# Kernel tuning notes

Hardware: AMD Instinct MI355X
Metric: run time of the kernel (lower is better)

Reference implementation:

```python
import jax, jax.numpy as jnp
import numpy as np
import math

B, N, D, H, L, F, K = 4, 256, 768, 32, 12, 3072, 128
HD = D // H
ATOM_TYPES = 64
EDGE_TYPES = ATOM_TYPES * ATOM_TYPES
BLOCKS = 1
SQRT_2PI = math.sqrt(2.0 * math.pi)


def _ln(x, g, b):
    m = jnp.mean(x, -1, keepdims=True)
    v = jnp.mean((x - m) ** 2, -1, keepdims=True)
    return (x - m) * jax.lax.rsqrt(v + 1e-5) * g + b


def _gelu(x):
    return jax.nn.gelu(x, approximate=False)


def setup_inputs():
    key = jax.random.key(0)
    ks = iter(jax.random.split(key, 64))
    def nrm(shape, s=0.02):
        return jax.random.normal(next(ks), shape, jnp.float32) * s
    inp = dict(
        atoms=jax.random.randint(next(ks), (B, N), 0, ATOM_TYPES),
        tags=jax.random.randint(next(ks), (B, N), 0, 3),
        pos=jax.random.normal(next(ks), (B, N, 3), jnp.float32) * 3.0,
        real_mask=jnp.ones((B, N), dtype=bool),
        atom_emb=nrm((ATOM_TYPES, D)),
        tag_emb=nrm((3, D)),
        gbf_means=jax.random.uniform(next(ks), (K,), jnp.float32, 0.0, 3.0),
        gbf_stds=jax.random.uniform(next(ks), (K,), jnp.float32, 0.0, 3.0),
        gbf_mul=jnp.ones((EDGE_TYPES, 1), jnp.float32),
        gbf_bias=jnp.zeros((EDGE_TYPES, 1), jnp.float32),
        bp_w1=nrm((K, K)), bp_b1=jnp.zeros((K,), jnp.float32),
        bp_w2=nrm((H, K)), bp_b2=jnp.zeros((H,), jnp.float32),
        ep_w=nrm((D, K)), ep_b=jnp.zeros((D,), jnp.float32),
        ln1_g=jnp.ones((L, D), jnp.float32), ln1_b=jnp.zeros((L, D), jnp.float32),
        wqkv=nrm((L, 3 * D, D)), bqkv=jnp.zeros((L, 3 * D), jnp.float32),
        wo=nrm((L, D, D)), bo=jnp.zeros((L, D), jnp.float32),
        ln2_g=jnp.ones((L, D), jnp.float32), ln2_b=jnp.zeros((L, D), jnp.float32),
        w1=nrm((L, F, D)), b1=jnp.zeros((L, F), jnp.float32),
        w2=nrm((L, D, F)), b2=jnp.zeros((L, D), jnp.float32),
        fln_g=jnp.ones((D,), jnp.float32), fln_b=jnp.zeros((D,), jnp.float32),
        en_w1=nrm((D, D)), en_b1=jnp.zeros((D,), jnp.float32),
        en_w2=nrm((1, D)), en_b2=jnp.zeros((1,), jnp.float32),
        eagg=nrm((3, 1), 0.01),
        nq_w=nrm((D, D)), nq_b=jnp.zeros((D,), jnp.float32),
        nk_w=nrm((D, D)), nk_b=jnp.zeros((D,), jnp.float32),
        nv_w=nrm((D, D)), nv_b=jnp.zeros((D,), jnp.float32),
        f1_w=nrm((1, D)), f1_b=jnp.zeros((1,), jnp.float32),
        f2_w=nrm((1, D)), f2_b=jnp.zeros((1,), jnp.float32),
        f3_w=nrm((1, D)), f3_b=jnp.zeros((1,), jnp.float32),
    )
    return inp


def _forward(atoms, tags, real_mask, pos, atom_emb, tag_emb, gbf_means, gbf_stds, gbf_mul, gbf_bias,
             bp_w1, bp_b1, bp_w2, bp_b2, ep_w, ep_b,
             ln1_g, ln1_b, wqkv, bqkv, wo, bo, ln2_g, ln2_b, w1, b1, w2, b2,
             fln_g, fln_b, en_w1, en_b1, en_w2, en_b2, eagg,
             nq_w, nq_b, nk_w, nk_b, nv_w, nv_b, f1_w, f1_b, f2_w, f2_b, f3_w, f3_b):
    pad = atoms == 0                                              # [B,N]
    # delta[b,i,j] = pos[b,j] - pos[b,i]  (matches pos.unsqueeze(1) - pos.unsqueeze(2))
    delta = pos[:, None, :, :] - pos[:, :, None, :]               # [B,N,N,3]
    sq = jnp.sum(delta * delta, axis=-1)
    dist = jnp.sqrt(jnp.maximum(sq, 1e-24))                       # safe norm, zero grad on diagonal
    delta = delta / (dist[..., None] + 1e-5)
    edge_type = atoms[:, :, None] * ATOM_TYPES + atoms[:, None, :]  # [B,N,N]
    # Gaussian basis layer
    mul = gbf_mul[edge_type]                                      # [B,N,N,1]
    add = gbf_bias[edge_type]                                     # [B,N,N,1]
    x = mul * dist[..., None] + add                               # [B,N,N,1] -> broadcast to K
    std = jnp.abs(gbf_stds) + 1e-5                                # [K]
    z = (x - gbf_means) / std
    gbf = jnp.exp(-0.5 * z * z) / (SQRT_2PI * std)                # [B,N,N,K]
    edge_feat = jnp.where(pad[:, None, :, None], 0.0, gbf)
    node = tag_emb[tags] + atom_emb[atoms] + (edge_feat.sum(-2) @ ep_w.T + ep_b)  # [B,N,D]
    bias = _gelu(gbf @ bp_w1.T + bp_b1) @ bp_w2.T + bp_b2         # [B,N,N,H]
    bias = jnp.transpose(bias, (0, 3, 1, 2))                      # [B,H,N,N]
    bias = jnp.where(pad[:, None, None, :], -jnp.inf, bias)
    scale = HD ** -0.5
    h = node
    for _ in range(BLOCKS):
        for l in range(L):
            r = h
            y = _ln(h, ln1_g[l], ln1_b[l])
            qkv = y @ wqkv[l].T + bqkv[l]
            q, k, v = jnp.split(qkv, 3, axis=-1)
            q = q.reshape(B, N, H, HD).transpose(0, 2, 1, 3) * scale
            k = k.reshape(B, N, H, HD).transpose(0, 2, 1, 3)
            v = v.reshape(B, N, H, HD).transpose(0, 2, 1, 3)
            a = jnp.einsum('bhid,bhjd->bhij', q, k) + bias
            a = jax.nn.softmax(a, axis=-1)
            o = jnp.einsum('bhij,bhjd->bhid', a, v).transpose(0, 2, 1, 3).reshape(B, N, D)
            h = r + (o @ wo[l].T + bo[l])
            r = h
            y = _ln(h, ln2_g[l], ln2_b[l])
            y = _gelu(y @ w1[l].T + b1[l]) @ w2[l].T + b2[l]
            h = r + y
    out = _ln(h, fln_g, fln_b)                                    # [B,N,D]
    # energy head (eval: no dropout)
    eng = _gelu(out @ en_w1.T + en_b1) @ en_w2.T + en_b2          # [B,N,1]
    eng = (eng * eagg[tags])[..., 0]                              # [B,N]
    omask = (tags > 0) & real_mask
    eng_output = (eng * omask).sum(-1)                            # [B]
    # node task head
    q = (out @ nq_w.T + nq_b).reshape(B, N, H, HD).transpose(0, 2, 1, 3) * scale
    k = (out @ nk_w.T + nk_b).reshape(B, N, H, HD).transpose(0, 2, 1, 3)
    v = (out @ nv_w.T + nv_b).reshape(B, N, H, HD).transpose(0, 2, 1, 3)
    a = jnp.einsum('bhid,bhjd->bhij', q, k) + bias
    a = jax.nn.softmax(a, axis=-1)                                # [B,H,N,N]
    # rot_attn_probs @ v, fused: [b,h,i,j]*[b,i,j,c]*[b,h,j,d] -> [b,i,c,h,d]
    xf = jnp.einsum('bhij,bijc,bhjd->bichd', a, delta, v).reshape(B, N, 3, D)
    f1 = xf[:, :, 0] @ f1_w.T + f1_b
    f2 = xf[:, :, 1] @ f2_w.T + f2_b
    f3 = xf[:, :, 2] @ f3_w.T + f3_b
    node_output = jnp.concatenate([f1, f2, f3], axis=-1)          # [B,N,3]
    return eng_output, node_output, omask[..., None]


def reference(atoms, tags, pos, real_mask, atom_emb, tag_emb, gbf_means, gbf_stds, gbf_mul, gbf_bias,
              bp_w1, bp_b1, bp_w2, bp_b2, ep_w, ep_b,
              ln1_g, ln1_b, wqkv, bqkv, wo, bo, ln2_g, ln2_b, w1, b1, w2, b2,
              fln_g, fln_b, en_w1, en_b1, en_w2, en_b2, eagg,
              nq_w, nq_b, nk_w, nk_b, nv_w, nv_b, f1_w, f1_b, f2_w, f2_b, f3_w, f3_b):
    return _forward(atoms, tags, real_mask, pos, atom_emb, tag_emb, gbf_means, gbf_stds, gbf_mul, gbf_bias,
                    bp_w1, bp_b1, bp_w2, bp_b2, ep_w, ep_b,
                    ln1_g, ln1_b, wqkv, bqkv, wo, bo, ln2_g, ln2_b, w1, b1, w2, b2,
                    fln_g, fln_b, en_w1, en_b1, en_w2, en_b2, eagg,
                    nq_w, nq_b, nk_w, nk_b, nv_w, nv_b, f1_w, f1_b, f2_w, f2_b, f3_w, f3_b)
```

## Files before the change

kernel.cpp:

```cpp
#include <hip/hip_runtime.h>
#include <math.h>

constexpr int B_ = 4, N_ = 256, D_ = 768, H_ = 32, HD_ = 24, L_ = 12, F_ = 3072, K_ = 128;
constexpr float SCALE_ = 0.20412414523193150f;
constexpr float ISQRT2_ = 0.70710678118654752f;

typedef short bf16x8 __attribute__((ext_vector_type(8)));
typedef float f32x4 __attribute__((ext_vector_type(4)));
typedef unsigned short u16x4 __attribute__((ext_vector_type(4)));
typedef unsigned short u16x8 __attribute__((ext_vector_type(8)));
typedef unsigned int u32x4 __attribute__((ext_vector_type(4)));

#define DEV __device__ __forceinline__
#define MFMA16(a, b, c) __builtin_amdgcn_mfma_f32_16x16x32_bf16(a, b, c, 0, 0, 0)

DEV void gload_lds16(const unsigned short* g, unsigned short* l) {
  __builtin_amdgcn_global_load_lds(
      (const __attribute__((address_space(1))) unsigned int*)(g),
      (__attribute__((address_space(3))) unsigned int*)(l), 16, 0, 0);
}

DEV float gelu_f(float x) { return 0.5f * x * (1.0f + erff(x * ISQRT2_)); }

DEV unsigned short f2bf(float f) {
  unsigned u = __float_as_uint(f);
  return (unsigned short)((u + 0x7FFFu + ((u >> 16) & 1u)) >> 16);
}
DEV float bf2f(unsigned short u) { return __uint_as_float(((unsigned)u) << 16); }
DEV unsigned packbf(float a, float b) {
  return (unsigned)f2bf(a) | ((unsigned)f2bf(b) << 16);
}
DEV bf16x8 u4_to_bf8(u32x4 x) { union { u32x4 a; bf16x8 b; } u; u.a = x; return u.b; }

DEV float breduce_sum(float v, float* sred, int tid) {
#pragma unroll
  for (int o = 32; o > 0; o >>= 1) v += __shfl_xor(v, o);
  if ((tid & 63) == 0) sred[tid >> 6] = v;
  __syncthreads();
  v = (sred[0] + sred[1]) + (sred[2] + sred[3]);
  __syncthreads();
  return v;
}

__global__ __launch_bounds__(256) void cast_one_kernel(
    const float* __restrict__ s, unsigned short* __restrict__ d, int n4) {
  const int i = blockIdx.x * 256 + threadIdx.x;
  if (i >= n4) return;
  const float4 v = ((const float4*)s)[i];
  u16x4 o = {f2bf(v.x), f2bf(v.y), f2bf(v.z), f2bf(v.w)};
  ((u16x4*)d)[i] = o;
}

__global__ __launch_bounds__(256) void castlayer_kernel(
    const float* __restrict__ wqkv, const float* __restrict__ wo,
    const float* __restrict__ w1, const float* __restrict__ w2,
    unsigned short* __restrict__ arena) {
  const int i = blockIdx.x * 256 + threadIdx.x;
  const float* s; int j;
  if (i < 442368) { s = wqkv; j = i; }
  else if (i < 589824) { s = wo; j = i - 442368; }
  else if (i < 1179648) { s = w1; j = i - 589824; }
  else { s = w2; j = i - 1179648; }
  const float4 v = ((const float4*)s)[j];
  u16x4 o = {f2bf(v.x), f2bf(v.y), f2bf(v.z), f2bf(v.w)};
  ((u16x4*)arena)[i] = o;
}

__global__ __launch_bounds__(256) void castheads_kernel(
    const float* __restrict__ a, const float* __restrict__ b,
    const float* __restrict__ c, const float* __restrict__ d,
    unsigned short* __restrict__ arena) {
  const int i = blockIdx.x * 256 + threadIdx.x;
  const int r = i / 147456;
  const int j = i - r * 147456;
  const float* s = (r == 0) ? a : (r == 1) ? b : (r == 2) ? c : d;
  const float4 v = ((const float4*)s)[j];
  u16x4 o = {f2bf(v.x), f2bf(v.y), f2bf(v.z), f2bf(v.w)};
  ((u16x4*)arena)[i] = o;
}

__global__ __launch_bounds__(256) void edge_pre_kernel(
    const int* __restrict__ atoms, const float* __restrict__ pos,
    const float* __restrict__ gbf_mul, const float* __restrict__ gbf_bias,
    const float* __restrict__ gbf_means, const float* __restrict__ gbf_stds,
    float* __restrict__ deltaw, float* __restrict__ xvalw, float* __restrict__ nsumw)
{
  const int tid = threadIdx.x;
  const int bi = blockIdx.x;
  const int b = bi >> 8;
  __shared__ float spos[3];
  __shared__ float sxv[256];
  __shared__ int   spad[256];
  __shared__ float red[256];
  if (tid < 3) spos[tid] = pos[(size_t)bi * 3 + tid];
  __syncthreads();
  {
    const int j = tid;
    const float px = pos[(size_t)(b * N_ + j) * 3 + 0];
    const float py = pos[(size_t)(b * N_ + j) * 3 + 1];
    const float pz = pos[(size_t)(b * N_ + j) * 3 + 2];
    const float dx = px - spos[0], dy = py - spos[1], dz = pz - spos[2];
    const float sq = dx * dx + dy * dy + dz * dz;
    const float dist = sqrtf(fmaxf(sq, 1e-24f));
    const float inv = 1.f / (dist + 1e-5f);
    const size_t e = (size_t)bi * N_ + j;
    deltaw[e * 3 + 0] = dx * inv;
    deltaw[e * 3 + 1] = dy * inv;
    deltaw[e * 3 + 2] = dz * inv;
    const int et = atoms[bi] * 64 + atoms[b * N_ + j];
    const float xv = gbf_mul[et] * dist + gbf_bias[et];
    xvalw[e] = xv;
    sxv[j] = xv;
    spad[j] = (atoms[b * N_ + j] == 0);
  }
  __syncthreads();
  const int k = tid & 127;
  const float mean = gbf_means[k];
  const float st = fabsf(gbf_stds[k]) + 1e-5f;
  const float istd = 1.f / st;
  const float coef = 0.39894228040143268f * istd;
  float acc = 0.f;
  const int jbase = tid >> 7;
  for (int t = 0; t < 128; ++t) {
    const int j = jbase + (t << 1);
    if (!spad[j]) {
      const float z = (sxv[j] - mean) * istd;
      acc += expf(-0.5f * z * z) * coef;
    }
  }
  red[tid] = acc;
  __syncthreads();
  if (tid < 128) nsumw[(size_t)bi * K_ + tid] = red[tid] + red[tid + 128];
}

__global__ __launch_bounds__(256) void bias_mfma_kernel(
    const float* __restrict__ xvalw, const int* __restrict__ atoms,
    const float* __restrict__ gbf_means, const float* __restrict__ gbf_stds,
    const unsigned short* __restrict__ w1b, const float* __restrict__ b1,
    const unsigned short* __restrict__ w2b, const float* __restrict__ b2,
    unsigned short* __restrict__ biasb)
{
  __shared__ __align__(16) unsigned short sw1[128 * 128];
  __shared__ __align__(16) unsigned short sw2[32 * 128];
  __shared__ float smean[128], sistd[128], scoef[128], sb1[128], sb2[32];
  const int tid = threadIdx.x;
  const int l = tid & 63;
  const int w = tid >> 6;
  const size_t e0 = (size_t)blockIdx.x * 64;
  const int bB = (int)(e0 >> 16);
  const int iI = (int)((e0 >> 8) & 255);
  const int j0 = (int)(e0 & 255);
  const int lr = l & 15;
  const int lg = l >> 4;

  {
    const int rin = l >> 4;
    const int slot = l & 15;
#pragma unroll
    for (int q = 0; q < 8; ++q) {
      const int rbase = w * 32 + q * 4;
      const int row = rbase + rin;
      const int gs = slot ^ (row & 15);
      gload_lds16(w1b + row * 128 + gs * 8, &sw1[rbase * 128]);
    }
#pragma unroll
    for (int q = 0; q < 2; ++q) {
      const int rbase = w * 8 + q * 4;
      const int row = rbase + rin;
      const int gs = slot ^ (row & 15);
      gload_lds16(w2b + row * 128 + gs * 8, &sw2[rbase * 128]);
    }
  }
  if (tid < 128) {
    const float st = fabsf(gbf_stds[tid]) + 1e-5f;
    const float is = 1.f / st;
    smean[tid] = gbf_means[tid];
    sistd[tid] = is;
    scoef[tid] = 0.39894228040143268f * is;
    sb1[tid] = b1[tid];
  } else if (tid < 160) {
    sb2[tid - 128] = b2[tid - 128];
  }
  const int el = w * 16 + lr;
  const float xv = xvalw[e0 + el];
  const bool padq = (atoms[bB * N_ + j0 + el] == 0);
  __syncthreads();

  bf16x8 bG[4];
#pragma unroll
  for (int ks = 0; ks < 4; ++ks) {
    u16x8 t;
#pragma unroll
    for (int j = 0; j < 8; ++j) {
      const int k = ks * 32 + lg * 8 + j;
      const float z = (xv - smean[k]) * sistd[k];
      t[j] = f2bf(__expf(-0.5f * z * z) * scoef[k]);
    }
    union { u16x8 a; bf16x8 b; } u; u.a = t;
    bG[ks] = u.b;
  }

  f32x4 accM[8];
#pragma unroll
  for (int f = 0; f < 8; ++f) accM[f] = (f32x4)0.f;
#pragma unroll
  for (int ks = 0; ks < 4; ++ks) {
#pragma unroll
    for (int f = 0; f < 8; ++f) {
      const int row = f * 16 + lr;
      const int sl = (ks * 4 + lg) ^ (row & 15);
      const bf16x8 aW = *(const bf16x8*)&sw1[row * 128 + (sl << 3)];
      accM[f] = MFMA16(aW, bG[ks], accM[f]);
    }
  }

  unsigned pm[8][2];
#pragma unroll
  for (int f = 0; f < 8; ++f) {
    float g[4];
#pragma unroll
    for (int r = 0; r < 4; ++r)
      g[r] = gelu_f(accM[f][r] + sb1[f * 16 + lg * 4 + r]);
    pm[f][0] = packbf(g[0], g[1]);
    pm[f][1] = packbf(g[2], g[3]);
  }

  f32x4 accH[2];
  accH[0] = (f32x4)0.f; accH[1] = (f32x4)0.f;
#pragma unroll
  for (int ks = 0; ks < 4; ++ks) {
    const int s0 = ((((lg << 1)) & 3) << 4) + lr;
    const int s1 = ((((lg << 1) + 1) & 3) << 4) + lr;
    const int sel = lg >> 1;
    const unsigned a0 = __shfl(pm[2 * ks][0], s0), b0 = __shfl(pm[2 * ks + 1][0], s0);
    const unsigned a1 = __shfl(pm[2 * ks][1], s0), b1v = __shfl(pm[2 * ks + 1][1], s0);
    const unsigned a2 = __shfl(pm[2 * ks][0], s1), b2v = __shfl(pm[2 * ks + 1][0], s1);
    const unsigned a3 = __shfl(pm[2 * ks][1], s1), b3v = __shfl(pm[2 * ks + 1][1], s1);
    u32x4 bw;
    bw.x = sel ? b0 : a0;
    bw.y = sel ? b1v : a1;
    bw.z = sel ? b2v : a2;
    bw.w = sel ? b3v : a3;
    const bf16x8 bMid = u4_to_bf8(bw);
#pragma unroll
    for (int hf = 0; hf < 2; ++hf) {
      const int row = hf * 16 + lr;
      const int sl = (ks * 4 + lg) ^ (row & 15);
      const bf16x8 aW2 = *(const bf16x8*)&sw2[row * 128 + (sl << 3)];
      accH[hf] = MFMA16(aW2, bMid, accH[hf]);
    }
  }

  const size_t obase = (((size_t)bB * H_) * N_ + iI) * N_ + j0 + el;
#pragma unroll
  for (int hf = 0; hf < 2; ++hf) {
#pragma unroll
    for (int r = 0; r < 4; ++r) {
      const int h = hf * 16 + lg * 4 + r;
      const unsigned short v = padq ? (unsigned short)0xFF80
                                    : f2bf(accH[hf][r] + sb2[h]);
      biasb[obase + (size_t)h * N_ * N_] = v;
    }
  }
}

__global__ __launch_bounds__(256) void node_init_kernel(
    const int* __restrict__ atoms, const int* __restrict__ tags,
    const float* __restrict__ atom_emb, const float* __restrict__ tag_emb,
    const float* __restrict__ nsumw, const float* __restrict__ ep_w,
    const float* __restrict__ ep_b, float* __restrict__ hbuf)
{
  const int bi = blockIdx.x;
  const int tid = threadIdx.x;
  __shared__ float ns[K_];
  if (tid < K_) ns[tid] = nsumw[(size_t)bi * K_ + tid];
  __syncthreads();
  const int at = atoms[bi], tg = tags[bi];
  for (int d = tid; d < D_; d += 256) {
    float acc = tag_emb[tg * D_ + d] + atom_emb[at * D_ + d] + ep_b[d];
    const float* w = ep_w + (size_t)d * K_;
#pragma unroll 8
    for (int kk = 0; kk < K_; ++kk) acc = fmaf(ns[kk], w[kk], acc);
    hbuf[(size_t)bi * D_ + d] = acc;
  }
}

__global__ __launch_bounds__(256) void ln_kernel(
    const float* __restrict__ x, const float* __restrict__ gg,
    const float* __restrict__ bb, unsigned short* __restrict__ y)
{
  const int bi = blockIdx.x;
  const int tid = threadIdx.x;
  __shared__ float sred[4];
  const float* row = x + (size_t)bi * D_;
  const float v0 = row[tid], v1 = row[tid + 256], v2 = row[tid + 512];
  float s = breduce_sum(v0 + v1 + v2, sred, tid);
  const float mean = s * (1.f / 768.f);
  const float d0 = v0 - mean, d1 = v1 - mean, d2 = v2 - mean;
  float q = breduce_sum(d0 * d0 + d1 * d1 + d2 * d2, sred, tid);
  const float inv = rsqrtf(q * (1.f / 768.f) + 1e-5f);
  unsigned short* out = y + (size_t)bi * D_;
  out[tid]       = f2bf(d0 * inv * gg[tid]       + bb[tid]);
  out[tid + 256] = f2bf(d1 * inv * gg[tid + 256] + bb[tid + 256]);
  out[tid + 512] = f2bf(d2 * inv * gg[tid + 512] + bb[tid + 512]);
}

template <int S>
__global__ __launch_bounds__(256) void reduce_ln_kernel(
    const float* __restrict__ P, const float* __restrict__ bias,
    float* __restrict__ hbuf, const float* __restrict__ gg,
    const float* __restrict__ bb, unsigned short* __restrict__ y)
{
  const int row = blockIdx.x;
  const int tid = threadIdx.x;
  __shared__ float sred[4];
  float h[3];
#pragma unroll
  for (int t = 0; t < 3; ++t) {
    const int c = tid + (t << 8);
    float s = bias[c];
#pragma unroll
    for (int z = 0; z < S; ++z)
      s += P[((size_t)z * (B_ * N_) + row) * 768 + c];
    const float hv = hbuf[(size_t)row * 768 + c] + s;
    hbuf[(size_t)row * 768 + c] = hv;
    h[t] = hv;
  }
  float sm = breduce_sum(h[0] + h[1] + h[2], sred, tid);
  const float mean = sm * (1.f / 768.f);
  const float d0 = h[0] - mean, d1 = h[1] - mean, d2 = h[2] - mean;
  float q = breduce_sum(d0 * d0 + d1 * d1 + d2 * d2, sred, tid);
  const float inv = rsqrtf(q * (1.f / 768.f) + 1e-5f);
  unsigned short* out = y + (size_t)row * 768;
  out[tid]       = f2bf(d0 * inv * gg[tid]       + bb[tid]);
  out[tid + 256] = f2bf(d1 * inv * gg[tid + 256] + bb[tid + 256]);
  out[tid + 512] = f2bf(d2 * inv * gg[tid + 512] + bb[tid + 512]);
}

template <int EPI, int OB>
__global__ __launch_bounds__(256) void gemm_mfma(
    const unsigned short* __restrict__ A, const unsigned short* __restrict__ W,
    const float* __restrict__ bias, const float* __restrict__ bias2,
    const float* __restrict__ bias3, const float* __restrict__ bias4,
    float* __restrict__ C, unsigned short* __restrict__ Cb,
    int M, int N, int K, int lda, int ldw)
{
  if (EPI == 4) {
    const int z = blockIdx.z;
    A += (size_t)z * K;
    W += (size_t)z * K;
    C += (size_t)z * M * N;
  }
  __shared__ __align__(16) unsigned short sA[2][64 * 64];
  __shared__ __align__(16) unsigned short sB[2][64 * 64];
  const int tid = threadIdx.x;
  const int l = tid & 63;
  const int w = tid >> 6;
  const int m0 = blockIdx.y * 64;
  const int n0 = blockIdx.x * 64;
  const int wm = w >> 1, wn = w & 1;
  const int lr = l & 15;
  const int lg = l >> 4;
  const int r0 = (w << 4) + (l >> 3);
  const int s0 = (l & 7) ^ (r0 & 7);

  f32x4 acc[2][2];
#pragma unroll
  for (int mi = 0; mi < 2; ++mi)
#pragma unroll
    for (int ni = 0; ni < 2; ++ni) acc[mi][ni] = (f32x4)0.f;

  auto stage = [&](int buf, int t) {
    const size_t kb = (size_t)t << 6;
    unsigned short* lA = &sA[buf][(w << 4) << 6];
    unsigned short* lB = &sB[buf][(w << 4) << 6];
    gload_lds16(A + (size_t)(m0 + r0) * lda + kb + (s0 << 3), lA);
    gload_lds16(A + (size_t)(m0 + r0 + 8) * lda + kb + (s0 << 3), lA + 8 * 64);
    gload_lds16(W + (size_t)(n0 + r0) * ldw + kb + (s0 << 3), lB);
    gload_lds16(W + (size_t)(n0 + r0 + 8) * ldw + kb + (s0 << 3), lB + 8 * 64);
  };

  stage(0, 0);
  const int nt = K >> 6;
  for (int t = 0; t < nt; ++t) {
    __syncthreads();
    if (t + 1 < nt) stage((t + 1) & 1, t + 1);
    const unsigned short* bA = sA[t & 1];
    const unsigned short* bBs = sB[t & 1];
    bf16x8 af[2][2], bfr[2][2];
#pragma unroll
    for (int mi = 0; mi < 2; ++mi) {
      const int row = (wm << 5) + (mi << 4) + lr;
#pragma unroll
      for (int kk = 0; kk < 2; ++kk) {
        const int sl = ((kk << 2) + lg) ^ (row & 7);
        af[mi][kk] = *(const bf16x8*)&bA[(row << 6) + (sl << 3)];
      }
    }
#pragma unroll
    for (int ni = 0; ni < 2; ++ni) {
      const int row = (wn << 5) + (ni << 4) + lr;
#pragma unroll
      for (int kk = 0; kk < 2; ++kk) {
        const int sl = ((kk << 2) + lg) ^ (row & 7);
        bfr[ni][kk] = *(const bf16x8*)&bBs[(row << 6) + (sl << 3)];
      }
    }
#pragma unroll
    for (int kk = 0; kk < 2; ++kk)
#pragma unroll
      for (int mi = 0; mi < 2; ++mi)
#pragma unroll
        for (int ni = 0; ni < 2; ++ni)
          acc[mi][ni] = MFMA16(af[mi][kk], bfr[ni][kk], acc[mi][ni]);
  }

#pragma unroll
  for (int mi = 0; mi < 2; ++mi)
#pragma unroll
    for (int ni = 0; ni < 2; ++ni) {
      const int n = n0 + (wn << 5) + (ni << 4) + lr;
      float bv = 0.f;
      int seg = 0;
      if (EPI == 3) {
        seg = n / 768;
        const float* bp = (seg == 0) ? bias : (seg == 1) ? bias2
                         : (seg == 2) ? bias3 : bias4;
        bv = bp[n - seg * 768];
      } else if (EPI != 4) {
        bv = bias[n];
      }
#pragma unroll
      for (int r = 0; r < 4; ++r) {
        const int m = m0 + (wm << 5) + (mi << 4) + lg * 4 + r;
        float v = acc[mi][ni][r] + bv;
        if (EPI == 1) v = gelu_f(v);
        if (EPI == 3 && seg == 3) v = gelu_f(v);
        if (OB) Cb[(size_t)m * N + n] = f2bf(v);
        else C[(size_t)m * N + n] = v;
      }
    }
}

template <bool PROBS>
__global__ __launch_bounds__(256) void attn_mfma_kernel(
    const unsigned short* __restrict__ Q, const unsigned short* __restrict__ Kp,
    const unsigned short* __restrict__ Vp, const int stride,
    const unsigned short* __restrict__ biasb, unsigned short* __restrict__ obuf,
    unsigned short* __restrict__ aprob)
{
  __shared__ __align__(16) unsigned short sK[256 * 40];
  __shared__ __align__(16) unsigned short sVt[32 * 264];
  __shared__ __align__(16) unsigned short sP[64 * 264];
  const int tid = threadIdx.x;
  const int l = tid & 63, w = tid >> 6;
  const int bh = blockIdx.x, b = bh >> 5, hh = bh & 31;
  const int i0 = blockIdx.y * 64;
  const int lr = l & 15, lg = l >> 4;

#pragma unroll
  for (int it = 0; it < 3; ++it) {
    const int c = tid + (it << 8);
    const int row = c / 3, part = c - row * 3;
    *(u16x8*)&sK[row * 40 + part * 8] =
        *(const u16x8*)&Kp[(size_t)(b * N_ + row) * stride + hh * HD_ + part * 8];
  }
  {
    u16x8 z = {0, 0, 0, 0, 0, 0, 0, 0};
    *(u16x8*)&sK[tid * 40 + 24] = z;
  }
  if (!PROBS) {
    const int j = tid;
    const unsigned short* vr = &Vp[(size_t)(b * N_ + j) * stride + hh * HD_];
    const u16x8 v0 = *(const u16x8*)vr;
    const u16x8 v1 = *(const u16x8*)(vr + 8);
    const u16x8 v2 = *(const u16x8*)(vr + 16);
#pragma unroll
    for (int d = 0; d < 8; ++d) {
      sVt[d * 264 + j] = v0[d];
      sVt[(8 + d) * 264 + j] = v1[d];
      sVt[(16 + d) * 264 + j] = v2[d];
    }
  }
  bf16x8 aQ;
  if (lg < 3) {
    const u16x8 q = *(const u16x8*)&Q[(size_t)(b * N_ + i0 + (w << 4) + lr) * stride + hh * HD_ + lg * 8];
    union { u16x8 a; bf16x8 b; } u; u.a = q;
    aQ = u.b;
  } else {
    bf16x8 t = {0, 0, 0, 0, 0, 0, 0, 0};
    aQ = t;
  }
  __syncthreads();

  f32x4 acc[16];
#pragma unroll
  for (int ni = 0; ni < 16; ++ni) {
    const bf16x8 bK = *(const bf16x8*)&sK[(ni * 16 + lr) * 40 + lg * 8];
    acc[ni] = MFMA16(aQ, bK, (f32x4)0.f);
  }

#pragma unroll
  for (int r = 0; r < 4; ++r) {
    const int iloc = (w << 4) + lg * 4 + r;
    const unsigned short* bp =
        &biasb[(((size_t)(b * H_ + hh)) * N_ + i0 + iloc) * N_ + lr];
    float mx = -INFINITY;
#pragma unroll
    for (int ni = 0; ni < 16; ++ni) {
      const float s = acc[ni][r] * SCALE_ + bf2f(bp[ni * 16]);
      acc[ni][r] = s;
      mx = fmaxf(mx, s);
    }
    mx = fmaxf(mx, __shfl_xor(mx, 1));
    mx = fmaxf(mx, __shfl_xor(mx, 2));
    mx = fmaxf(mx, __shfl_xor(mx, 4));
    mx = fmaxf(mx, __shfl_xor(mx, 8));
    float sum = 0.f;
#pragma unroll
    for (int ni = 0; ni < 16; ++ni) {
      const float e = expf(acc[ni][r] - mx);
      acc[ni][r] = e;
      sum += e;
    }
    sum += __shfl_xor(sum, 1);
    sum += __shfl_xor(sum, 2);
    sum += __shfl_xor(sum, 4);
    sum += __shfl_xor(sum, 8);
    const float inv = 1.f / sum;
#pragma unroll
    for (int ni = 0; ni < 16; ++ni)
      sP[iloc * 264 + ni * 16 + lr] = f2bf(acc[ni][r] * inv);
  }
  __syncthreads();

  if (PROBS) {
#pragma unroll
    for (int it = 0; it < 8; ++it) {
      const int idx = tid + it * 256;
      const int row = idx >> 5, c = idx & 31;
      *(u16x8*)&aprob[(((size_t)(b * H_ + hh)) * N_ + i0 + row) * N_ + c * 8] =
          *(const u16x8*)&sP[row * 264 + c * 8];
    }
  } else {
    f32x4 accO[2];
    accO[0] = (f32x4)0.f; accO[1] = (f32x4)0.f;
#pragma unroll
    for (int ks = 0; ks < 8; ++ks) {
      const bf16x8 aP = *(const bf16x8*)&sP[((w << 4) + lr) * 264 + ks * 32 + lg * 8];
      const bf16x8 bV0 = *(const bf16x8*)&sVt[lr * 264 + ks * 32 + lg * 8];
      const bf16x8 bV1 = *(const bf16x8*)&sVt[(16 + lr) * 264 + ks * 32 + lg * 8];
      accO[0] = MFMA16(aP, bV0, accO[0]);
      accO[1] = MFMA16(aP, bV1, accO[1]);
    }
#pragma unroll
    for (int ni = 0; ni < 2; ++ni) {
      const int n = ni * 16 + lr;
      if (n < HD_) {
#pragma unroll
        for (int r = 0; r < 4; ++r) {
          const int i = i0 + (w << 4) + lg * 4 + r;
          obuf[(size_t)(b * N_ + i) * D_ + hh * HD_ + n] = f2bf(accO[ni][r]);
        }
      }
    }
  }
}

__global__ __launch_bounds__(256) void engnode_kernel(
    const unsigned short* __restrict__ t1, const int stride,
    const float* __restrict__ en_w2, const float* __restrict__ en_b2,
    const float* __restrict__ eagg, const int* __restrict__ tags,
    float* __restrict__ engpn)
{
  const int bi = blockIdx.x;
  const int tid = threadIdx.x;
  __shared__ float sred[4];
  const unsigned short* row = t1 + (size_t)bi * stride;
  float acc = bf2f(row[tid]) * en_w2[tid] + bf2f(row[tid + 256]) * en_w2[tid + 256] +
              bf2f(row[tid + 512]) * en_w2[tid + 512];
  acc = breduce_sum(acc, sred, tid);
  if (tid == 0) {
    const int tg = tags[bi];
    engpn[bi] = (tg > 0) ? (acc + en_b2[0]) * eagg[tg] : 0.f;
  }
}

__global__ __launch_bounds__(256) void engsum_omask_kernel(
    const float* __restrict__ engpn, const int* __restrict__ tags,
    float* __restrict__ out)
{
  const int bid = blockIdx.x;
  const int tid = threadIdx.x;
  if (bid < 4) {
    __shared__ float sred[4];
    float v = breduce_sum(engpn[bid * N_ + tid], sred, tid);
    if (tid == 0) out[bid] = v;
  } else {
    const int idx = (bid - 4) * 256 + tid;
    out[4 + B_ * N_ * 3 + idx] = (tags[idx] > 0) ? 1.f : 0.f;
  }
}

__global__ __launch_bounds__(256) void wv_kernel(
    const unsigned short* __restrict__ vn, const int stride,
    const float* __restrict__ f1w, const float* __restrict__ f2w,
    const float* __restrict__ f3w, float* __restrict__ wv)
{
  const int idx = blockIdx.x * 256 + threadIdx.x;
  const int j = idx & 255;
  const int hh = (idx >> 8) & 31;
  const int b = (idx >> 13) & 3;
  const int c = idx >> 15;
  const float* fw = (c == 0) ? f1w : ((c == 1) ? f2w : f3w);
  const unsigned short* vrow = vn + (size_t)(b * N_ + j) * stride + hh * HD_;
  const u16x8 v0 = *(const u16x8*)vrow;
  const u16x8 v1 = *(const u16x8*)(vrow + 8);
  const u16x8 v2 = *(const u16x8*)(vrow + 16);
  float acc = 0.f;
#pragma unroll
  for (int d = 0; d < 8; ++d) {
    acc = fmaf(bf2f(v0[d]), fw[hh * HD_ + d], acc);
    acc = fmaf(bf2f(v1[d]), fw[hh * HD_ + 8 + d], acc);
    acc = fmaf(bf2f(v2[d]), fw[hh * HD_ + 16 + d], acc);
  }
  wv[idx] = acc;
}

__global__ __launch_bounds__(256) void nodeout_kernel(
    const unsigned short* __restrict__ aprob, const float* __restrict__ wv,
    const float* __restrict__ deltaw, const float* __restrict__ f1b,
    const float* __restrict__ f2b, const float* __restrict__ f3b,
    float* __restrict__ out)
{
  const int bi = blockIdx.x;
  const int c = blockIdx.y;
  const int tid = threadIdx.x;
  const int b = bi >> 8;
  const int i = bi & 255;
  __shared__ float sred[4];
  const unsigned short* ap = aprob + (((size_t)b * H_) * N_ + i) * N_ + tid;
  const float* wvp = wv + ((size_t)(c * B_ + b) * H_) * N_ + tid;
  float s = 0.f;
  for (int hh = 0; hh < H_; ++hh)
    s = fmaf(bf2f(ap[(size_t)hh * N_ * N_]), wvp[(size_t)hh * N_], s);
  s *= deltaw[((size_t)bi * N_ + tid) * 3 + c];
  s = breduce_sum(s, sred, tid);
  if (tid == 0) {
    const float fb = (c == 0) ? f1b[0] : ((c == 1) ? f2b[0] : f3b[0]);
    out[4 + bi * 3 + c] = s + fb;
  }
}

extern "C" void kernel_launch(void* const* d_in, const int* in_sizes, int n_in,
                              void* d_out, int out_size, void* d_ws, size_t ws_size,
                              hipStream_t stream) {
  (void)in_sizes; (void)n_in; (void)out_size; (void)ws_size;
  const int*   atoms     = (const int*)  d_in[0];
  const int*   tags      = (const int*)  d_in[1];
  const float* pos       = (const float*)d_in[2];
  const float* atom_emb  = (const float*)d_in[4];
  const float* tag_emb   = (const float*)d_in[5];
  const float* gbf_means = (const float*)d_in[6];
  const float* gbf_stds  = (const float*)d_in[7];
  const float* gbf_mul   = (const float*)d_in[8];
  const float* gbf_bias  = (const float*)d_in[9];
  const float* bp_w1     = (const float*)d_in[10];
  const float* bp_b1     = (const float*)d_in[11];
  const float* bp_w2     = (const float*)d_in[12];
  const float* bp_b2     = (const float*)d_in[13];
  const float* ep_w      = (const float*)d_in[14];
  const float* ep_b      = (const float*)d_in[15];
  const float* ln1_g     = (const float*)d_in[16];
  const float* ln1_b     = (const float*)d_in[17];
  const float* wqkv      = (const float*)d_in[18];
  const float* bqkv      = (const float*)d_in[19];
  const float* wo        = (const float*)d_in[20];
  const float* bo        = (const float*)d_in[21];
  const float* ln2_g     = (const float*)d_in[22];
  const float* ln2_b     = (const float*)d_in[23];
  const float* w1        = (const float*)d_in[24];
  const float* b1        = (const float*)d_in[25];
  const float* w2        = (const float*)d_in[26];
  const float* b2        = (const float*)d_in[27];
  const float* fln_g     = (const float*)d_in[28];
  const float* fln_b     = (const float*)d_in[29];
  const float* en_w1     = (const float*)d_in[30];
  const float* en_b1     = (const float*)d_in[31];
  const float* en_w2     = (const float*)d_in[32];
  const float* en_b2     = (const float*)d_in[33];
  const float* eagg      = (const float*)d_in[34];
  const float* nq_w      = (const float*)d_in[35];
  const float* nq_b      = (const float*)d_in[36];
  const float* nk_w      = (const float*)d_in[37];
  const float* nk_b      = (const float*)d_in[38];
  const float* nv_w      = (const float*)d_in[39];
  const float* nv_b      = (const float*)d_in[40];
  const float* f1_w      = (const float*)d_in[41];
  const float* f1_b      = (const float*)d_in[42];
  const float* f2_w      = (const float*)d_in[43];
  const float* f2_b      = (const float*)d_in[44];
  const float* f3_w      = (const float*)d_in[45];
  const float* f3_b      = (const float*)d_in[46];

  char* wsB = (char*)d_ws;
  size_t off = 0;
  auto alloc = [&](size_t bytes) {
    void* p = wsB + off;
    off = (off + bytes + 255) & ~(size_t)255;
    return p;
  };
  unsigned short* biasb   = (unsigned short*)alloc((size_t)B_ * H_ * N_ * N_ * 2);
  unsigned short* aprobb  = (unsigned short*)alloc((size_t)B_ * H_ * N_ * N_ * 2);
  float*          deltaw  = (float*)alloc((size_t)B_ * N_ * N_ * 3 * 4);
  float*          xvalw   = (float*)alloc((size_t)B_ * N_ * N_ * 4);
  float*          nsumw   = (float*)alloc((size_t)B_ * N_ * K_ * 4);
  float*          hbuf    = (float*)alloc((size_t)B_ * N_ * D_ * 4);
  unsigned short* qkvb    = (unsigned short*)alloc((size_t)B_ * N_ * 3 * D_ * 2);
  unsigned short* qn4b    = (unsigned short*)alloc((size_t)B_ * N_ * 3072 * 2);
  unsigned short* ybf     = (unsigned short*)alloc((size_t)B_ * N_ * D_ * 2);
  unsigned short* obf     = (unsigned short*)alloc((size_t)B_ * N_ * D_ * 2);
  unsigned short* midbf   = (unsigned short*)alloc((size_t)B_ * N_ * F_ * 2);
  unsigned short* outbf   = (unsigned short*)alloc((size_t)B_ * N_ * D_ * 2);
  unsigned short* arena   = (unsigned short*)alloc((size_t)7077888 * 2);
  unsigned short* headsb  = (unsigned short*)alloc((size_t)2359296 * 2);
  unsigned short* bw1b    = (unsigned short*)alloc((size_t)K_ * K_ * 2);
  unsigned short* bw2b    = (unsigned short*)alloc((size_t)H_ * K_ * 2);
  float*          wopart  = (float*)alloc((size_t)2 * B_ * N_ * D_ * 4);
  float*          ffpart  = (float*)alloc((size_t)4 * B_ * N_ * D_ * 4);
  float*          wvb     = (float*)alloc((size_t)3 * B_ * H_ * N_ * 4);
  float*          engpn   = (float*)alloc((size_t)B_ * N_ * 4);

  const int BN = B_ * N_;
  float* outp = (float*)d_out;
  const size_t OQKV = 0, OWO = 1769472, OW1 = 2359296, OW2 = 4718592;

  edge_pre_kernel<<<BN, 256, 0, stream>>>(atoms, pos, gbf_mul, gbf_bias,
                                          gbf_means, gbf_stds, deltaw, xvalw, nsumw);
  cast_one_kernel<<<16, 256, 0, stream>>>(bp_w1, bw1b, 4096);
  cast_one_kernel<<<4, 256, 0, stream>>>(bp_w2, bw2b, 1024);
  bias_mfma_kernel<<<B_ * N_ * N_ / 64, 256, 0, stream>>>(
      xvalw, atoms, gbf_means, gbf_stds, bw1b, bp_b1, bw2b, bp_b2, biasb);
  node_init_kernel<<<BN, 256, 0, stream>>>(atoms, tags, atom_emb, tag_emb,
                                           nsumw, ep_w, ep_b, hbuf);
  ln_kernel<<<BN, 256, 0, stream>>>(hbuf, ln1_g, ln1_b, ybf);

  for (int l = 0; l < L_; ++l) {
    castlayer_kernel<<<6912, 256, 0, stream>>>(
        wqkv + (size_t)l * 3 * D_ * D_, wo + (size_t)l * D_ * D_,
        w1 + (size_t)l * F_ * D_, w2 + (size_t)l * D_ * F_, arena);
    gemm_mfma<0, 1><<<dim3(36, 16), 256, 0, stream>>>(
        ybf, arena + OQKV, bqkv + (size_t)l * 3 * D_, nullptr, nullptr, nullptr,
        nullptr, qkvb, BN, 3 * D_, D_, D_, D_);
    attn_mfma_kernel<false><<<dim3(B_ * H_, 4), 256, 0, stream>>>(
        qkvb, qkvb + D_, qkvb + 2 * D_, 3 * D_, biasb, obf, nullptr);
    gemm_mfma<4, 0><<<dim3(12, 16, 2), 256, 0, stream>>>(
        obf, arena + OWO, nullptr, nullptr, nullptr, nullptr,
        wopart, nullptr, BN, D_, 384, D_, D_);
    reduce_ln_kernel<2><<<BN, 256, 0, stream>>>(
        wopart, bo + (size_t)l * D_, hbuf, ln2_g + (size_t)l * D_,
        ln2_b + (size_t)l * D_, ybf);
    gemm_mfma<1, 1><<<dim3(48, 16), 256, 0, stream>>>(
        ybf, arena + OW1, b1 + (size_t)l * F_, nullptr, nullptr, nullptr,
        nullptr, midbf, BN, F_, D_, D_, D_);
    gemm_mfma<4, 0><<<dim3(12, 16, 4), 256, 0, stream>>>(
        midbf, arena + OW2, nullptr, nullptr, nullptr, nullptr,
        ffpart, nullptr, BN, D_, 768, F_, F_);
    const bool last = (l == L_ - 1);
    reduce_ln_kernel<4><<<BN, 256, 0, stream>>>(
        ffpart, b2 + (size_t)l * D_, hbuf,
        last ? fln_g : ln1_g + (size_t)(l + 1) * D_,
        last ? fln_b : ln1_b + (size_t)(l + 1) * D_,
        last ? outbf : ybf);
  }

  castheads_kernel<<<2304, 256, 0, stream>>>(nq_w, nk_w, nv_w, en_w1, headsb);

  gemm_mfma<3, 1><<<dim3(48, 16), 256, 0, stream>>>(
      outbf, headsb, nq_b, nk_b, nv_b, en_b1,
      nullptr, qn4b, BN, 3072, D_, D_, D_);

  attn_mfma_kernel<true><<<dim3(B_ * H_, 4), 256, 0, stream>>>(
      qn4b, qn4b + 768, qn4b + 1536, 3072, biasb, nullptr, aprobb);
  wv_kernel<<<3 * B_ * H_ * N_ / 256, 256, 0, stream>>>(
      qn4b + 1536, 3072, f1_w, f2_w, f3_w, wvb);
  nodeout_kernel<<<dim3(BN, 3), 256, 0, stream>>>(aprobb, wvb, deltaw,
                                                  f1_b, f2_b, f3_b, outp);

  engnode_kernel<<<BN, 256, 0, stream>>>(qn4b + 2304, 3072, en_w2, en_b2,
                                         eagg, tags, engpn);
  engsum_omask_kernel<<<8, 256, 0, stream>>>(engpn, tags, outp);
}
```

Before: 1.078 ms.

## Widen weight casts, defer softmax normalization, fuse nodeout channels, use fast exp

The weight cast kernels now handle eight floats per thread with 16-byte stores and half as many blocks. The attention kernel uses __expf and, on the non-probability path, applies the 1/sum normalization to the output accumulators instead of to each probability. nodeout_kernel computes all three channels in one block, so each aprob row is read once instead of three times. edge_pre_kernel also switches to __expf, which adds small precision differences in the Gaussian features and the softmax.

```diff
diff --git a/kernel.cpp b/kernel.cpp
--- a/kernel.cpp
+++ b/kernel.cpp
@@ -55,28 +55,32 @@
     const float* __restrict__ wqkv, const float* __restrict__ wo,
     const float* __restrict__ w1, const float* __restrict__ w2,
     unsigned short* __restrict__ arena) {
-  const int i = blockIdx.x * 256 + threadIdx.x;
-  const float* s; int j;
-  if (i < 442368) { s = wqkv; j = i; }
-  else if (i < 589824) { s = wo; j = i - 442368; }
-  else if (i < 1179648) { s = w1; j = i - 589824; }
-  else { s = w2; j = i - 1179648; }
-  const float4 v = ((const float4*)s)[j];
-  u16x4 o = {f2bf(v.x), f2bf(v.y), f2bf(v.z), f2bf(v.w)};
-  ((u16x4*)arena)[i] = o;
+  const unsigned i = blockIdx.x * 256 + threadIdx.x;
+  const float* s; unsigned j;
+  if (i < 221184u) { s = wqkv; j = i; }
+  else if (i < 294912u) { s = wo; j = i - 221184u; }
+  else if (i < 589824u) { s = w1; j = i - 294912u; }
+  else { s = w2; j = i - 589824u; }
+  const float4 a = ((const float4*)s)[2u * j];
+  const float4 b = ((const float4*)s)[2u * j + 1u];
+  u16x8 o = {f2bf(a.x), f2bf(a.y), f2bf(a.z), f2bf(a.w),
+             f2bf(b.x), f2bf(b.y), f2bf(b.z), f2bf(b.w)};
+  ((u16x8*)arena)[i] = o;
 }
 
 __global__ __launch_bounds__(256) void castheads_kernel(
     const float* __restrict__ a, const float* __restrict__ b,
     const float* __restrict__ c, const float* __restrict__ d,
     unsigned short* __restrict__ arena) {
-  const int i = blockIdx.x * 256 + threadIdx.x;
-  const int r = i / 147456;
-  const int j = i - r * 147456;
+  const unsigned i = blockIdx.x * 256 + threadIdx.x;
+  const unsigned r = i / 73728u;
+  const unsigned j = i - r * 73728u;
   const float* s = (r == 0) ? a : (r == 1) ? b : (r == 2) ? c : d;
-  const float4 v = ((const float4*)s)[j];
-  u16x4 o = {f2bf(v.x), f2bf(v.y), f2bf(v.z), f2bf(v.w)};
-  ((u16x4*)arena)[i] = o;
+  const float4 a0 = ((const float4*)s)[2u * j];
+  const float4 a1 = ((const float4*)s)[2u * j + 1u];
+  u16x8 o = {f2bf(a0.x), f2bf(a0.y), f2bf(a0.z), f2bf(a0.w),
+             f2bf(a1.x), f2bf(a1.y), f2bf(a1.z), f2bf(a1.w)};
+  ((u16x8*)arena)[i] = o;
 }
 
 __global__ __launch_bounds__(256) void edge_pre_kernel(
@@ -125,7 +129,7 @@
     const int j = jbase + (t << 1);
     if (!spad[j]) {
       const float z = (sxv[j] - mean) * istd;
-      acc += expf(-0.5f * z * z) * coef;
+      acc += __expf(-0.5f * z * z) * coef;
     }
   }
   red[tid] = acc;
@@ -500,6 +504,7 @@
     acc[ni] = MFMA16(aQ, bK, (f32x4)0.f);
   }
 
+  float invr[4];
 #pragma unroll
   for (int r = 0; r < 4; ++r) {
     const int iloc = (w << 4) + lg * 4 + r;
@@ -519,7 +524,7 @@
     float sum = 0.f;
 #pragma unroll
     for (int ni = 0; ni < 16; ++ni) {
-      const float e = expf(acc[ni][r] - mx);
+      const float e = __expf(acc[ni][r] - mx);
       acc[ni][r] = e;
       sum += e;
     }
@@ -528,9 +533,11 @@
     sum += __shfl_xor(sum, 4);
     sum += __shfl_xor(sum, 8);
     const float inv = 1.f / sum;
+    invr[r] = inv;
 #pragma unroll
     for (int ni = 0; ni < 16; ++ni)
-      sP[iloc * 264 + ni * 16 + lr] = f2bf(acc[ni][r] * inv);
+      sP[iloc * 264 + ni * 16 + lr] = f2bf(PROBS ? acc[ni][r] * inv
+                                                 : acc[ni][r]);
   }
   __syncthreads();
 
@@ -560,7 +567,7 @@
 #pragma unroll
         for (int r = 0; r < 4; ++r) {
           const int i = i0 + (w << 4) + lg * 4 + r;
-          obuf[(size_t)(b * N_ + i) * D_ + hh * HD_ + n] = f2bf(accO[ni][r]);
+          obuf[(size_t)(b * N_ + i) * D_ + hh * HD_ + n] = f2bf(accO[ni][r] * invr[r]);
         }
       }
     }
@@ -634,21 +641,32 @@
     float* __restrict__ out)
 {
   const int bi = blockIdx.x;
-  const int c = blockIdx.y;
   const int tid = threadIdx.x;
   const int b = bi >> 8;
   const int i = bi & 255;
   __shared__ float sred[4];
   const unsigned short* ap = aprob + (((size_t)b * H_) * N_ + i) * N_ + tid;
-  const float* wvp = wv + ((size_t)(c * B_ + b) * H_) * N_ + tid;
-  float s = 0.f;
-  for (int hh = 0; hh < H_; ++hh)
-    s = fmaf(bf2f(ap[(size_t)hh * N_ * N_]), wvp[(size_t)hh * N_], s);
-  s *= deltaw[((size_t)bi * N_ + tid) * 3 + c];
-  s = breduce_sum(s, sred, tid);
+  const float* wv0 = wv + ((size_t)(0 * B_ + b) * H_) * N_ + tid;
+  const float* wv1 = wv + ((size_t)(1 * B_ + b) * H_) * N_ + tid;
+  const float* wv2 = wv + ((size_t)(2 * B_ + b) * H_) * N_ + tid;
+  float s0 = 0.f, s1 = 0.f, s2 = 0.f;
+  for (int hh = 0; hh < H_; ++hh) {
+    const float p = bf2f(ap[(size_t)hh * N_ * N_]);
+    s0 = fmaf(p, wv0[(size_t)hh * N_], s0);
+    s1 = fmaf(p, wv1[(size_t)hh * N_], s1);
+    s2 = fmaf(p, wv2[(size_t)hh * N_], s2);
+  }
+  const float* dl = &deltaw[((size_t)bi * N_ + tid) * 3];
+  s0 *= dl[0];
+  s1 *= dl[1];
+  s2 *= dl[2];
+  s0 = breduce_sum(s0, sred, tid);
+  s1 = breduce_sum(s1, sred, tid);
+  s2 = breduce_sum(s2, sred, tid);
   if (tid == 0) {
-    const float fb = (c == 0) ? f1b[0] : ((c == 1) ? f2b[0] : f3b[0]);
-    out[4 + bi * 3 + c] = s + fb;
+    out[4 + bi * 3 + 0] = s0 + f1b[0];
+    out[4 + bi * 3 + 1] = s1 + f2b[0];
+    out[4 + bi * 3 + 2] = s2 + f3b[0];
   }
 }
 
@@ -746,7 +764,7 @@
   ln_kernel<<<BN, 256, 0, stream>>>(hbuf, ln1_g, ln1_b, ybf);
 
   for (int l = 0; l < L_; ++l) {
-    castlayer_kernel<<<6912, 256, 0, stream>>>(
+    castlayer_kernel<<<3456, 256, 0, stream>>>(
         wqkv + (size_t)l * 3 * D_ * D_, wo + (size_t)l * D_ * D_,
         w1 + (size_t)l * F_ * D_, w2 + (size_t)l * D_ * F_, arena);
     gemm_mfma<0, 1><<<dim3(36, 16), 256, 0, stream>>>(
@@ -774,7 +792,7 @@
         last ? outbf : ybf);
   }
 
-  castheads_kernel<<<2304, 256, 0, stream>>>(nq_w, nk_w, nv_w, en_w1, headsb);
+  castheads_kernel<<<1152, 256, 0, stream>>>(nq_w, nk_w, nv_w, en_w1, headsb);
 
   gemm_mfma<3, 1><<<dim3(48, 16), 256, 0, stream>>>(
       outbf, headsb, nq_b, nk_b, nv_b, en_b1,
@@ -784,8 +802,8 @@
       qn4b, qn4b + 768, qn4b + 1536, 3072, biasb, nullptr, aprobb);
   wv_kernel<<<3 * B_ * H_ * N_ / 256, 256, 0, stream>>>(
       qn4b + 1536, 3072, f1_w, f2_w, f3_w, wvb);
-  nodeout_kernel<<<dim3(BN, 3), 256, 0, stream>>>(aprobb, wvb, deltaw,
-                                                  f1_b, f2_b, f3_b, outp);
+  nodeout_kernel<<<BN, 256, 0, stream>>>(aprobb, wvb, deltaw,
+                                         f1_b, f2_b, f3_b, outp);
 
   engnode_kernel<<<BN, 256, 0, stream>>>(qn4b + 2304, 3072, en_w2, en_b2,
                                          eagg, tags, engpn);
```

After: 1.020 ms. 5.4% less time.
